# Performance work log

Measured on AMD Instinct MI355X. Metric: run time of the kernel, lower is better.

Reference implementation:

```python
import jax, jax.numpy as jnp
import numpy as np

N = 50000      # nodes
E = 800000     # edges (before self loops)
IN = 128       # input_dim
ED = 16        # edge_dim
HID = 32       # hidden_dim (per-head out_channels)
H = 4          # heads
OUT = 64       # output_dim
NEG = 0.1      # negative_slope
EPS = 1e-5     # batchnorm eps


def setup_inputs() -> dict:
    key = jax.random.key(0)
    ks = jax.random.split(key, 32)
    s = 0.1
    p = {}
    p["x"] = jax.random.normal(ks[0], (N, IN), jnp.float32)
    p["edge_index"] = jax.random.randint(ks[1], (2, E), 0, N, dtype=jnp.int32)
    p["edge_attr"] = jax.random.normal(ks[2], (E, ED), jnp.float32)
    # input embed: Linear(IN, HID) + BatchNorm1d (eval-mode running stats)
    p["W0"] = jax.random.normal(ks[3], (HID, IN), jnp.float32) * s
    p["b0"] = jnp.zeros((HID,), jnp.float32)
    p["bn_g"] = jnp.ones((HID,), jnp.float32)
    p["bn_b"] = jnp.zeros((HID,), jnp.float32)
    p["bn_m"] = jnp.zeros((HID,), jnp.float32)
    p["bn_v"] = jnp.ones((HID,), jnp.float32)
    # two GATv2Conv layers: lin_l, lin_r [H*HID, HID] (+bias), lin_edge [H*HID, ED] (no bias),
    # att [H, HID], out bias [HID] (concat=False)
    k = 4
    for l in range(2):
        p[f"Wl{l}"] = jax.random.normal(ks[k + 0], (H * HID, HID), jnp.float32) * s
        p[f"bl{l}"] = jnp.zeros((H * HID,), jnp.float32)
        p[f"Wr{l}"] = jax.random.normal(ks[k + 1], (H * HID, HID), jnp.float32) * s
        p[f"br{l}"] = jnp.zeros((H * HID,), jnp.float32)
        p[f"We{l}"] = jax.random.normal(ks[k + 2], (H * HID, ED), jnp.float32) * s
        p[f"att{l}"] = jax.random.normal(ks[k + 3], (H, HID), jnp.float32) * s
        p[f"bias{l}"] = jnp.zeros((HID,), jnp.float32)
        k += 4
    p["Wout"] = jax.random.normal(ks[k], (OUT, HID), jnp.float32) * s
    p["bout"] = jnp.zeros((OUT,), jnp.float32)
    return p


def _gatv2(x, src, dst, eattr, Wl, bl, Wr, br, We, att, bias):
    # x: [N, HID]; src/dst: [Et]; eattr: [Et, ED]
    xl = (x @ Wl.T + bl).reshape(N, H, HID)   # source transform
    xr = (x @ Wr.T + br).reshape(N, H, HID)   # target transform
    ea = (eattr @ We.T).reshape(-1, H, HID)   # edge transform
    m = jax.nn.leaky_relu(xl[src] + xr[dst] + ea, NEG)   # [Et, H, HID]
    alpha = jnp.einsum('ehc,hc->eh', m, att)             # [Et, H]
    amax = jax.ops.segment_max(alpha, dst, num_segments=N)  # every node has a self loop
    ex = jnp.exp(alpha - amax[dst])
    den = jax.ops.segment_sum(ex, dst, num_segments=N)
    w = ex / den[dst]                                    # segment softmax [Et, H]
    out = jax.ops.segment_sum(xl[src] * w[:, :, None], dst, num_segments=N)  # [N, H, HID]
    return out.mean(axis=1) + bias                       # concat=False -> mean heads


def reference(x, edge_index, edge_attr,
              W0, b0, bn_g, bn_b, bn_m, bn_v,
              Wl0, bl0, Wr0, br0, We0, att0, bias0,
              Wl1, bl1, Wr1, br1, We1, att1, bias1,
              Wout, bout):
    src, dst = edge_index[0], edge_index[1]
    # input embed: Linear + BatchNorm1d(eval) + LeakyReLU(0.1)
    e = x @ W0.T + b0
    e = (e - bn_m) / jnp.sqrt(bn_v + EPS) * bn_g + bn_b
    e = jax.nn.leaky_relu(e, NEG)
    # add self loops once (same both layers): fill_value='mean' => per-dst mean edge_attr
    cnt = jax.ops.segment_sum(jnp.ones((E,), jnp.float32), dst, num_segments=N)
    loop_attr = jax.ops.segment_sum(edge_attr, dst, num_segments=N) / jnp.maximum(cnt, 1.0)[:, None]
    ar = jnp.arange(N, dtype=src.dtype)
    src_f = jnp.concatenate([src, ar])
    dst_f = jnp.concatenate([dst, ar])
    ea_f = jnp.concatenate([edge_attr, loop_attr], axis=0)
    h = _gatv2(e, src_f, dst_f, ea_f, Wl0, bl0, Wr0, br0, We0, att0, bias0)
    h = _gatv2(h, src_f, dst_f, ea_f, Wl1, bl1, Wr1, br1, We1, att1, bias1)
    return jax.nn.leaky_relu(h @ Wout.T + bout, NEG)
```

## Files before the change

### kernel.cpp

```cpp
#include <hip/hip_runtime.h>
#include <hip/hip_fp16.h>
#include <math.h>

#define NN   50000
#define EE   800000
#define IND  128
#define EDD  16
#define HIDD 32
#define NH   4
#define HC   128
#define OUTD 64
#define NEG  0.1f
#define BN_EPS 1e-5f
#define LOG2E 1.44269504088896340736f

typedef __attribute__((ext_vector_type(2))) float v2f;
typedef __attribute__((ext_vector_type(2))) _Float16 v2h;

#if defined(__has_builtin)
#  if __has_builtin(__builtin_amdgcn_fdot2)
#    define HAVE_FDOT2 1
#  else
#    define HAVE_FDOT2 0
#  endif
#else
#  define HAVE_FDOT2 0
#endif

__device__ __forceinline__ float lrelu(float x) { return fmaxf(x, NEG * x); }
__device__ __forceinline__ v2f lrelu2(v2f v) { return __builtin_elementwise_max(v, v * NEG); }
__device__ __forceinline__ float2 unpk(float f) {
    return __half22float2(__builtin_bit_cast(__half2, f));
}

#define DPPADD(p, CTRL) do {                                                     \
    int _t = __builtin_amdgcn_update_dpp(0, __builtin_bit_cast(int, (p)),        \
                                         (CTRL), 0xF, 0xF, true);                \
    (p) += __builtin_bit_cast(float, _t);                                        \
} while (0)

__global__ void fold_kernel(const float* __restrict__ W0, const float* __restrict__ b0,
                            const float* __restrict__ g, const float* __restrict__ bb,
                            const float* __restrict__ bm, const float* __restrict__ bv,
                            const float* __restrict__ Wl0, const float* __restrict__ Wr0,
                            const float* __restrict__ Wl1, const float* __restrict__ Wr1,
                            const float* __restrict__ We0, const float* __restrict__ We1,
                            float* __restrict__ w0t, float* __restrict__ b0f,
                            float* __restrict__ wlt0, float* __restrict__ wrt0,
                            float* __restrict__ wlt1, float* __restrict__ wrt1,
                            __half2* __restrict__ weh0, __half2* __restrict__ weh1) {
    int tid = threadIdx.x;
    for (int idx = tid; idx < IND * HIDD; idx += 256) {
        int k = idx >> 5, c = idx & 31;
        float s = g[c] * (1.0f / sqrtf(bv[c] + BN_EPS));
        w0t[idx] = W0[c * IND + k] * s;
    }
    if (tid < HIDD) {
        float s = g[tid] * (1.0f / sqrtf(bv[tid] + BN_EPS));
        b0f[tid] = (b0[tid] - bm[tid]) * s + bb[tid];
    }
    for (int idx = tid; idx < HIDD * HC; idx += 256) {
        int k = idx >> 7, c = idx & 127;
        wlt0[idx] = Wl0[c * HIDD + k];
        wrt0[idx] = Wr0[c * HIDD + k];
        wlt1[idx] = Wl1[c * HIDD + k];
        wrt1[idx] = Wr1[c * HIDD + k];
    }
    for (int idx = tid; idx < HC * 8; idx += 256) {
        int c = idx >> 3, k = idx & 7;
        weh0[idx] = __floats2half2_rn(We0[c * EDD + 2 * k], We0[c * EDD + 2 * k + 1]);
        weh1[idx] = __floats2half2_rn(We1[c * EDD + 2 * k], We1[c * EDD + 2 * k + 1]);
    }
}

__global__ void count_embed_kernel(const int* __restrict__ ei, int* __restrict__ cnt,
                                   int* __restrict__ rank,
                                   const float* __restrict__ x,
                                   const float* __restrict__ w0t, const float* __restrict__ b0f,
                                   const float* __restrict__ wlt, const float* __restrict__ bl,
                                   const float* __restrict__ wrt, const float* __restrict__ br,
                                   __half2* __restrict__ xl, float* __restrict__ xr) {
    if (blockIdx.x < EE / 256) {
        int e = blockIdx.x * 256 + threadIdx.x;
        rank[e] = atomicAdd(&cnt[(unsigned)ei[EE + e] << 4], 1);
        return;
    }
    int tid = threadIdx.x;
    int n0 = (blockIdx.x - EE / 256) * 8;
    __shared__ float sx[8 * IND];
    __shared__ float se[8][HIDD];
    *(float4*)(sx + tid * 4) = *(const float4*)(x + (size_t)n0 * IND + tid * 4);
    __syncthreads();
    {
        int r = tid >> 5, c = tid & 31;
        float acc = b0f[c];
        const float* xrow = sx + r * IND;
        #pragma unroll 8
        for (int k = 0; k < IND; k++) acc += xrow[k] * w0t[k * HIDD + c];
        se[r][c] = lrelu(acc);
    }
    __syncthreads();
    int mat = tid >> 7, grp = (tid >> 6) & 1, pr = tid & 63;
    int c0 = 2 * pr;
    const float* WT = mat ? wrt : wlt;
    const float* b  = mat ? br : bl;
    v2f bv2 = (v2f){b[c0], b[c0 + 1]};
    v2f a0 = bv2, a1 = bv2, a2 = bv2, a3 = bv2;
    int nb = grp * 4;
    #pragma unroll
    for (int k = 0; k < HIDD; k++) {
        v2f wk = *(const v2f*)(WT + k * HC + c0);
        a0 += wk * se[nb + 0][k]; a1 += wk * se[nb + 1][k];
        a2 += wk * se[nb + 2][k]; a3 += wk * se[nb + 3][k];
    }
    if (mat == 0) {
        xl[((unsigned)(n0 + nb + 0) << 6) + pr] = __floats2half2_rn(a0.x, a0.y);
        xl[((unsigned)(n0 + nb + 1) << 6) + pr] = __floats2half2_rn(a1.x, a1.y);
        xl[((unsigned)(n0 + nb + 2) << 6) + pr] = __floats2half2_rn(a2.x, a2.y);
        xl[((unsigned)(n0 + nb + 3) << 6) + pr] = __floats2half2_rn(a3.x, a3.y);
    } else {
        *(float2*)(xr + ((unsigned)(n0 + nb + 0) << 7) + c0) = make_float2(a0.x, a0.y);
        *(float2*)(xr + ((unsigned)(n0 + nb + 1) << 7) + c0) = make_float2(a1.x, a1.y);
        *(float2*)(xr + ((unsigned)(n0 + nb + 2) << 7) + c0) = make_float2(a2.x, a2.y);
        *(float2*)(xr + ((unsigned)(n0 + nb + 3) << 7) + c0) = make_float2(a3.x, a3.y);
    }
}

__global__ void scan1_kernel(const int* cnt, int* pre, int* bsum) {
    int i = blockIdx.x * 1024 + threadIdx.x;
    int lane = threadIdx.x & 63, wid = threadIdx.x >> 6;
    __shared__ int wsum[16];
    int v = (i < NN) ? cnt[(unsigned)i << 4] : 0;
    int s = v;
    #pragma unroll
    for (int off = 1; off < 64; off <<= 1) {
        int t = __shfl_up(s, off);
        if (lane >= off) s += t;
    }
    if (lane == 63) wsum[wid] = s;
    __syncthreads();
    if (wid == 0) {
        int ws = (lane < 16) ? wsum[lane] : 0;
        #pragma unroll
        for (int off = 1; off < 16; off <<= 1) {
            int t = __shfl_up(ws, off);
            if (lane >= off) ws += t;
        }
        if (lane < 16) wsum[lane] = ws;
    }
    __syncthreads();
    int woff = (wid > 0) ? wsum[wid - 1] : 0;
    if (i < NN) pre[i] = woff + s - v;
    if (threadIdx.x == 1023) bsum[blockIdx.x] = wsum[15];
}

__global__ void scan3_kernel(int* rowstart, const int* pre, const int* bsum, int nb) {
    __shared__ int boff_s;
    if (threadIdx.x < 64) {
        int lane = threadIdx.x;
        int v = (lane < nb) ? bsum[lane] : 0;
        int s = v;
        #pragma unroll
        for (int off = 1; off < 64; off <<= 1) {
            int t = __shfl_up(s, off);
            if (lane >= off) s += t;
        }
        if (lane == (int)blockIdx.x) boff_s = s - v;
    }
    __syncthreads();
    int i = blockIdx.x * 1024 + threadIdx.x;
    if (i < NN) rowstart[i] = pre[i] + boff_s;
    if (i == 0) rowstart[NN] = EE;
}

__global__ void scatter_kernel(const int* __restrict__ ei, const int* __restrict__ rowstart,
                               const int* __restrict__ rank, const float* __restrict__ eattr,
                               int* __restrict__ csr_src, __half2* __restrict__ ea16) {
    int e = blockIdx.x * blockDim.x + threadIdx.x;
    if (e >= EE) return;
    int d = ei[EE + e];
    int pos = rowstart[d] + rank[e];
    csr_src[pos] = ei[e];
    const float4* src = (const float4*)(eattr + ((size_t)e << 4));
    float4 q0 = src[0], q1 = src[1], q2 = src[2], q3 = src[3];
    __half2 h[8];
    h[0] = __floats2half2_rn(q0.x, q0.y); h[1] = __floats2half2_rn(q0.z, q0.w);
    h[2] = __floats2half2_rn(q1.x, q1.y); h[3] = __floats2half2_rn(q1.z, q1.w);
    h[4] = __floats2half2_rn(q2.x, q2.y); h[5] = __floats2half2_rn(q2.z, q2.w);
    h[6] = __floats2half2_rn(q3.x, q3.y); h[7] = __floats2half2_rn(q3.z, q3.w);
    float4* dst = (float4*)(ea16 + ((size_t)pos << 3));
    dst[0] = *(float4*)&h[0];
    dst[1] = *(float4*)&h[4];
}

__global__ void lin_kernel(const float* __restrict__ f,
                           const float* __restrict__ wlt, const float* __restrict__ bl,
                           const float* __restrict__ wrt, const float* __restrict__ br,
                           __half2* __restrict__ xl, float* __restrict__ xr) {
    int tid = threadIdx.x;
    int n0 = blockIdx.x * 8;
    __shared__ float se[8][HIDD];
    se[tid >> 5][tid & 31] = f[((unsigned)(n0 + (tid >> 5)) << 5) + (tid & 31)];
    __syncthreads();
    int mat = tid >> 7, grp = (tid >> 6) & 1, pr = tid & 63;
    int c0 = 2 * pr;
    const float* WT = mat ? wrt : wlt;
    const float* b  = mat ? br : bl;
    v2f bv2 = (v2f){b[c0], b[c0 + 1]};
    v2f a0 = bv2, a1 = bv2, a2 = bv2, a3 = bv2;
    int nb = grp * 4;
    #pragma unroll
    for (int k = 0; k < HIDD; k++) {
        v2f wk = *(const v2f*)(WT + k * HC + c0);
        a0 += wk * se[nb + 0][k]; a1 += wk * se[nb + 1][k];
        a2 += wk * se[nb + 2][k]; a3 += wk * se[nb + 3][k];
    }
    if (mat == 0) {
        xl[((unsigned)(n0 + nb + 0) << 6) + pr] = __floats2half2_rn(a0.x, a0.y);
        xl[((unsigned)(n0 + nb + 1) << 6) + pr] = __floats2half2_rn(a1.x, a1.y);
        xl[((unsigned)(n0 + nb + 2) << 6) + pr] = __floats2half2_rn(a2.x, a2.y);
        xl[((unsigned)(n0 + nb + 3) << 6) + pr] = __floats2half2_rn(a3.x, a3.y);
    } else {
        *(float2*)(xr + ((unsigned)(n0 + nb + 0) << 7) + c0) = make_float2(a0.x, a0.y);
        *(float2*)(xr + ((unsigned)(n0 + nb + 1) << 7) + c0) = make_float2(a1.x, a1.y);
        *(float2*)(xr + ((unsigned)(n0 + nb + 2) << 7) + c0) = make_float2(a2.x, a2.y);
        *(float2*)(xr + ((unsigned)(n0 + nb + 3) << 7) + c0) = make_float2(a3.x, a3.y);
    }
}

template<bool OUTHEAD>
__global__ void gat_fused_kernel(const __half2* __restrict__ xl, const float* __restrict__ xr,
                                 const __half2* __restrict__ ea16,
                                 const float* __restrict__ We,
                                 const __half2* __restrict__ weh,
                                 const float* __restrict__ att,
                                 const int* __restrict__ rowstart, const int* __restrict__ csr_src,
                                 const float* __restrict__ bias,
                                 const float* __restrict__ Wout, const float* __restrict__ bout,
                                 float* __restrict__ out) {
    int n = (blockIdx.x * blockDim.x + threadIdx.x) >> 6;
    int lane = threadIdx.x & 63;
    if (n >= NN) return;
    n = __builtin_amdgcn_readfirstlane(n);
    int start = __builtin_amdgcn_readfirstlane(rowstart[n]);
    int end   = __builtin_amdgcn_readfirstlane(rowstart[n + 1]);
    int deg = end - start;
    int c0 = 2 * lane;

    __half2 xLh = xl[((unsigned)n << 6) + lane];
    v2f xrv = *(const v2f*)(xr + ((unsigned)n << 7) + c0);
    v2f attv = *(const v2f*)(att + c0) * LOG2E;

#if HAVE_FDOT2
    (void)We;
    v2h wh0[8], wh1[8];
    {
        const float4* pw = (const float4*)(weh + (size_t)c0 * 8);
        float4 q0 = pw[0], q1 = pw[1], q2 = pw[2], q3 = pw[3];
        float t[16];
        *(float4*)(t)      = q0; *(float4*)(t + 4)  = q1;
        *(float4*)(t + 8)  = q2; *(float4*)(t + 12) = q3;
        #pragma unroll
        for (int k = 0; k < 8; k++) {
            wh0[k] = __builtin_bit_cast(v2h, t[k]);
            wh1[k] = __builtin_bit_cast(v2h, t[8 + k]);
        }
    }
    auto proj = [&](float4 r0, float4 r1) -> v2f {
        float e[8];
        *(float4*)(e) = r0; *(float4*)(e + 4) = r1;
        float a0 = 0.f, a1 = 0.f;
        #pragma unroll
        for (int k = 0; k < 8; k++) {
            v2h ek = __builtin_bit_cast(v2h, e[k]);
            a0 = __builtin_amdgcn_fdot2(ek, wh0[k], a0, false);
            a1 = __builtin_amdgcn_fdot2(ek, wh1[k], a1, false);
        }
        return (v2f){a0, a1};
    };
#else
    (void)weh;
    v2f wv[16];
    {
        const float* ra = We + c0 * EDD;
        const float* rb = ra + EDD;
        float4 a0 = *(const float4*)(ra),     a1 = *(const float4*)(ra + 4);
        float4 a2 = *(const float4*)(ra + 8), a3 = *(const float4*)(ra + 12);
        float4 b0 = *(const float4*)(rb),     b1 = *(const float4*)(rb + 4);
        float4 b2 = *(const float4*)(rb + 8), b3 = *(const float4*)(rb + 12);
        wv[0]=(v2f){a0.x,b0.x}; wv[1]=(v2f){a0.y,b0.y}; wv[2]=(v2f){a0.z,b0.z}; wv[3]=(v2f){a0.w,b0.w};
        wv[4]=(v2f){a1.x,b1.x}; wv[5]=(v2f){a1.y,b1.y}; wv[6]=(v2f){a1.z,b1.z}; wv[7]=(v2f){a1.w,b1.w};
        wv[8]=(v2f){a2.x,b2.x}; wv[9]=(v2f){a2.y,b2.y}; wv[10]=(v2f){a2.z,b2.z}; wv[11]=(v2f){a2.w,b2.w};
        wv[12]=(v2f){a3.x,b3.x}; wv[13]=(v2f){a3.y,b3.y}; wv[14]=(v2f){a3.z,b3.z}; wv[15]=(v2f){a3.w,b3.w};
    }
    auto proj = [&](float4 r0, float4 r1) -> v2f {
        float2 t0 = unpk(r0.x), t1 = unpk(r0.y), t2 = unpk(r0.z), t3 = unpk(r0.w);
        float2 t4 = unpk(r1.x), t5 = unpk(r1.y), t6 = unpk(r1.z), t7 = unpk(r1.w);
        return wv[0]*t0.x  + wv[1]*t0.y  + wv[2]*t1.x  + wv[3]*t1.y
             + wv[4]*t2.x  + wv[5]*t2.y  + wv[6]*t3.x  + wv[7]*t3.y
             + wv[8]*t4.x  + wv[9]*t4.y  + wv[10]*t5.x + wv[11]*t5.y
             + wv[12]*t6.x + wv[13]*t6.y + wv[14]*t7.x + wv[15]*t7.y;
    };
#endif

    float lh = 0.f;
    v2f acc   = (v2f){0.f, 0.f};
    v2f easum = (v2f){0.f, 0.f};

    auto proc = [&](v2f xv, v2f ea) {
        easum += ea;
        v2f z  = xv + xrv + ea;
        v2f mm = lrelu2(z);
        v2f pp = mm * attv;
        float p = pp.x + pp.y;
        DPPADD(p, 0xB1);
        DPPADD(p, 0x4E);
        DPPADD(p, 0x124);
        DPPADD(p, 0x128);
        float w = exp2f(p);
        lh  += w;
        acc += xv * w;
    };

    #define GATHER(i0, S0, S1, S2, S3, X0, X1, X2, X3, E0, E1, E2, E3) do {           \
        __half2 xh0 = xl[((unsigned)(S0) << 6) + lane];                                \
        __half2 xh1 = xl[((unsigned)(S1) << 6) + lane];                                \
        __half2 xh2 = xl[((unsigned)(S2) << 6) + lane];                                \
        __half2 xh3 = xl[((unsigned)(S3) << 6) + lane];                                \
        const float4* ep = (const float4*)(ea16 + ((size_t)(unsigned)(i0) << 3));      \
        float4 r00 = ep[0], r01 = ep[1], r10 = ep[2], r11 = ep[3];                     \
        float4 r20 = ep[4], r21 = ep[5], r30 = ep[6], r31 = ep[7];                     \
        E0 = proj(r00, r01); E1 = proj(r10, r11);                                      \
        E2 = proj(r20, r21); E3 = proj(r30, r31);                                      \
        float2 xf;                                                                     \
        xf = __half22float2(xh0); X0 = (v2f){xf.x, xf.y};                              \
        xf = __half22float2(xh1); X1 = (v2f){xf.x, xf.y};                              \
        xf = __half22float2(xh2); X2 = (v2f){xf.x, xf.y};                              \
        xf = __half22float2(xh3); X3 = (v2f){xf.x, xf.y};                              \
    } while (0)

    int i = start;
    int nf = deg >> 2;
    if (nf > 0) {
        int v0 = csr_src[i],     v1 = csr_src[i + 1],
            v2 = csr_src[i + 2], v3 = csr_src[i + 3];
        int j4 = (i + 4 > EE - 4) ? (EE - 4) : (i + 4);
        int u0 = csr_src[j4],     u1 = csr_src[j4 + 1],
            u2 = csr_src[j4 + 2], u3 = csr_src[j4 + 3];
        int s0 = __builtin_amdgcn_readfirstlane(v0), s1 = __builtin_amdgcn_readfirstlane(v1);
        int s2 = __builtin_amdgcn_readfirstlane(v2), s3 = __builtin_amdgcn_readfirstlane(v3);
        v2f A0x, A1x, A2x, A3x, A0e, A1e, A2e, A3e;
        GATHER(i, s0, s1, s2, s3, A0x, A1x, A2x, A3x, A0e, A1e, A2e, A3e);
        for (int k = 1; k < nf; k++) {
            int jn = i + 4 * (k + 1);
            jn = (jn > EE - 4) ? (EE - 4) : jn;
            int w0 = csr_src[jn],     w1 = csr_src[jn + 1],
                w2 = csr_src[jn + 2], w3 = csr_src[jn + 3];
            int t0 = __builtin_amdgcn_readfirstlane(u0), t1 = __builtin_amdgcn_readfirstlane(u1);
            int t2 = __builtin_amdgcn_readfirstlane(u2), t3 = __builtin_amdgcn_readfirstlane(u3);
            v2f B0x, B1x, B2x, B3x, B0e, B1e, B2e, B3e;
            GATHER(i + 4 * k, t0, t1, t2, t3, B0x, B1x, B2x, B3x, B0e, B1e, B2e, B3e);
            proc(A0x, A0e); proc(A1x, A1e); proc(A2x, A2e); proc(A3x, A3e);
            A0x = B0x; A1x = B1x; A2x = B2x; A3x = B3x;
            A0e = B0e; A1e = B1e; A2e = B2e; A3e = B3e;
            u0 = w0; u1 = w1; u2 = w2; u3 = w3;
        }
        proc(A0x, A0e); proc(A1x, A1e); proc(A2x, A2e); proc(A3x, A3e);
        i += 4 * nf;
    }
    int rem = end - i;
    if (rem > 0) {
        v2f Tx[3], Te[3];
        int sA = __builtin_amdgcn_readfirstlane(csr_src[i]);
        int sB = (rem > 1) ? __builtin_amdgcn_readfirstlane(csr_src[i + 1]) : sA;
        int sC = (rem > 2) ? __builtin_amdgcn_readfirstlane(csr_src[i + 2]) : sA;
        __half2 xh0 = xl[((unsigned)sA << 6) + lane];
        __half2 xh1 = xl[((unsigned)sB << 6) + lane];
        __half2 xh2 = xl[((unsigned)sC << 6) + lane];
        const float4* ep = (const float4*)(ea16 + ((size_t)(unsigned)i << 3));
        int lim2 = (rem > 1) ? 2 : 0, lim4 = (rem > 2) ? 4 : 0;
        float4 r00 = ep[0], r01 = ep[1];
        float4 r10 = ep[lim2], r11 = ep[lim2 + 1];
        float4 r20 = ep[lim4], r21 = ep[lim4 + 1];
        float2 xf;
        xf = __half22float2(xh0); Tx[0] = (v2f){xf.x, xf.y};
        xf = __half22float2(xh1); Tx[1] = (v2f){xf.x, xf.y};
        xf = __half22float2(xh2); Tx[2] = (v2f){xf.x, xf.y};
        Te[0] = proj(r00, r01); Te[1] = proj(r10, r11); Te[2] = proj(r20, r21);
        proc(Tx[0], Te[0]);
        if (rem > 1) proc(Tx[1], Te[1]);
        if (rem > 2) proc(Tx[2], Te[2]);
    }

    {
        float invdeg = 1.0f / (float)(deg > 0 ? deg : 1);
        float2 xf = __half22float2(xLh);
        proc((v2f){xf.x, xf.y}, easum * invdeg);
    }

    float inv = 1.0f / lh;
    float acc0 = acc.x * inv, acc1 = acc.y * inv;
    acc0 += __shfl_xor(acc0, 16); acc0 += __shfl_xor(acc0, 32);
    acc1 += __shfl_xor(acc1, 16); acc1 += __shfl_xor(acc1, 32);

    if (!OUTHEAD) {
        if (lane < 16) {
            float2 o = make_float2(acc0 * 0.25f + bias[2 * lane],
                                   acc1 * 0.25f + bias[2 * lane + 1]);
            *(float2*)(out + ((unsigned)n << 5) + 2 * lane) = o;
        }
    } else {
        __shared__ __align__(16) float sh[4][HIDD];
        int w = threadIdx.x >> 6;
        if (lane < 16) {
            sh[w][2 * lane]     = acc0 * 0.25f + bias[2 * lane];
            sh[w][2 * lane + 1] = acc1 * 0.25f + bias[2 * lane + 1];
        }
        float a = bout[lane];
        const float4* wr4 = (const float4*)(Wout + lane * HIDD);
        const float4* sv4 = (const float4*)(&sh[w][0]);
        #pragma unroll
        for (int k = 0; k < 8; k++) {
            float4 s4 = sv4[k], w4 = wr4[k];
            a += s4.x * w4.x + s4.y * w4.y + s4.z * w4.z + s4.w * w4.w;
        }
        out[((unsigned)n << 6) + lane] = lrelu(a);
    }
    #undef GATHER
}

extern "C" void kernel_launch(void* const* d_in, const int* in_sizes, int n_in,
                              void* d_out, int out_size, void* d_ws, size_t ws_size,
                              hipStream_t stream) {
    const float* x     = (const float*)d_in[0];
    const int*   ei    = (const int*)  d_in[1];
    const float* eattr = (const float*)d_in[2];
    const float* W0    = (const float*)d_in[3];
    const float* b0    = (const float*)d_in[4];
    const float* bn_g  = (const float*)d_in[5];
    const float* bn_b  = (const float*)d_in[6];
    const float* bn_m  = (const float*)d_in[7];
    const float* bn_v  = (const float*)d_in[8];
    const float* Wl[2]   = { (const float*)d_in[9],  (const float*)d_in[16] };
    const float* bl[2]   = { (const float*)d_in[10], (const float*)d_in[17] };
    const float* Wr[2]   = { (const float*)d_in[11], (const float*)d_in[18] };
    const float* br[2]   = { (const float*)d_in[12], (const float*)d_in[19] };
    const float* We[2]   = { (const float*)d_in[13], (const float*)d_in[20] };
    const float* att[2]  = { (const float*)d_in[14], (const float*)d_in[21] };
    const float* bias[2] = { (const float*)d_in[15], (const float*)d_in[22] };
    const float* Wout  = (const float*)d_in[23];
    const float* bout  = (const float*)d_in[24];
    float* out = (float*)d_out;

    const int NB = (NN + 1023) / 1024;
    char* p = (char*)d_ws;
    auto carve = [&](size_t bytes) { char* r = p; p += (bytes + 255) & ~(size_t)255; return r; };
    float*   h1       = (float*)  carve((size_t)NN * HIDD * 4);
    __half2* xl       = (__half2*)carve((size_t)NN * HC * 2);
    float*   xr       = (float*)  carve((size_t)NN * HC * 4);
    int*     cnt      = (int*)    carve((size_t)NN * 64);
    int*     rank     = (int*)    carve((size_t)EE * 4);
    int*     pre      = (int*)    carve((size_t)NN * 4);
    int*     bsum     = (int*)    carve((size_t)64 * 4);
    int*     rowstart = (int*)    carve((size_t)(NN + 1) * 4);
    int*     csr_src  = (int*)    carve((size_t)EE * 4);
    __half2* ea16     = (__half2*)carve((size_t)EE * EDD * 2);
    float*   w0t      = (float*)  carve((size_t)IND * HIDD * 4);
    float*   b0f      = (float*)  carve((size_t)HIDD * 4);
    float*   wlt0     = (float*)  carve((size_t)HIDD * HC * 4);
    float*   wrt0     = (float*)  carve((size_t)HIDD * HC * 4);
    float*   wlt1     = (float*)  carve((size_t)HIDD * HC * 4);
    float*   wrt1     = (float*)  carve((size_t)HIDD * HC * 4);
    __half2* weh0     = (__half2*)carve((size_t)HC * 8 * 4);
    __half2* weh1     = (__half2*)carve((size_t)HC * 8 * 4);

    hipMemsetAsync(cnt, 0, (size_t)NN * 64, stream);

    fold_kernel<<<1, 256, 0, stream>>>(W0, b0, bn_g, bn_b, bn_m, bn_v,
                                       Wl[0], Wr[0], Wl[1], Wr[1], We[0], We[1],
                                       w0t, b0f, wlt0, wrt0, wlt1, wrt1, weh0, weh1);
    count_embed_kernel<<<EE / 256 + NN / 8, 256, 0, stream>>>(
        ei, cnt, rank, x, w0t, b0f, wlt0, bl[0], wrt0, br[0], xl, xr);
    scan1_kernel<<<NB, 1024, 0, stream>>>(cnt, pre, bsum);
    scan3_kernel<<<NB, 1024, 0, stream>>>(rowstart, pre, bsum, NB);
    scatter_kernel<<<(EE + 255) / 256, 256, 0, stream>>>(ei, rowstart, rank, eattr,
                                                         csr_src, ea16);

    gat_fused_kernel<false><<<(NN * 64) / 256, 256, 0, stream>>>(
        xl, xr, ea16, We[0], weh0, att[0], rowstart, csr_src, bias[0], nullptr, nullptr, h1);

    lin_kernel<<<NN / 8, 256, 0, stream>>>(h1, wlt1, bl[1], wrt1, br[1], xl, xr);
    gat_fused_kernel<true><<<(NN * 64) / 256, 256, 0, stream>>>(
        xl, xr, ea16, We[1], weh1, att[1], rowstart, csr_src, bias[1], Wout, bout, out);
}
```

Baseline: 465.6 us.

## Keep edge attributes in original order and gather them by edge id

Converts edge attributes to fp16 in the counting pass in original edge order, and has the scatter pass write only (source, edge id) pairs into the CSR. The GAT kernels then fetch each edge's attribute row through the stored edge id instead of reading them contiguously in CSR order. This removes the scattered 32-byte attribute write from the scatter kernel, but it turns the contiguous attribute reads in both GAT layers into random gathers and doubles the size of the CSR index reads.

Measured after the change: 448.4 us. 1.04x faster.

```diff
diff --git a/kernel.cpp b/kernel.cpp
--- a/kernel.cpp
+++ b/kernel.cpp
@@ -75,6 +75,8 @@
 
 __global__ void count_embed_kernel(const int* __restrict__ ei, int* __restrict__ cnt,
                                    int* __restrict__ rank,
+                                   const float* __restrict__ eattr,
+                                   __half2* __restrict__ ea16,
                                    const float* __restrict__ x,
                                    const float* __restrict__ w0t, const float* __restrict__ b0f,
                                    const float* __restrict__ wlt, const float* __restrict__ bl,
@@ -82,7 +84,17 @@
                                    __half2* __restrict__ xl, float* __restrict__ xr) {
     if (blockIdx.x < EE / 256) {
         int e = blockIdx.x * 256 + threadIdx.x;
+        const float4* src = (const float4*)(eattr + ((size_t)e << 4));
+        float4 q0 = src[0], q1 = src[1], q2 = src[2], q3 = src[3];
         rank[e] = atomicAdd(&cnt[(unsigned)ei[EE + e] << 4], 1);
+        __half2 h[8];
+        h[0] = __floats2half2_rn(q0.x, q0.y); h[1] = __floats2half2_rn(q0.z, q0.w);
+        h[2] = __floats2half2_rn(q1.x, q1.y); h[3] = __floats2half2_rn(q1.z, q1.w);
+        h[4] = __floats2half2_rn(q2.x, q2.y); h[5] = __floats2half2_rn(q2.z, q2.w);
+        h[6] = __floats2half2_rn(q3.x, q3.y); h[7] = __floats2half2_rn(q3.z, q3.w);
+        float4* dst = (float4*)(ea16 + ((size_t)e << 3));
+        dst[0] = *(float4*)&h[0];
+        dst[1] = *(float4*)&h[4];
         return;
     }
     int tid = threadIdx.x;
@@ -174,23 +186,12 @@
 }
 
 __global__ void scatter_kernel(const int* __restrict__ ei, const int* __restrict__ rowstart,
-                               const int* __restrict__ rank, const float* __restrict__ eattr,
-                               int* __restrict__ csr_src, __half2* __restrict__ ea16) {
+                               const int* __restrict__ rank, int2* __restrict__ csr2) {
     int e = blockIdx.x * blockDim.x + threadIdx.x;
     if (e >= EE) return;
     int d = ei[EE + e];
     int pos = rowstart[d] + rank[e];
-    csr_src[pos] = ei[e];
-    const float4* src = (const float4*)(eattr + ((size_t)e << 4));
-    float4 q0 = src[0], q1 = src[1], q2 = src[2], q3 = src[3];
-    __half2 h[8];
-    h[0] = __floats2half2_rn(q0.x, q0.y); h[1] = __floats2half2_rn(q0.z, q0.w);
-    h[2] = __floats2half2_rn(q1.x, q1.y); h[3] = __floats2half2_rn(q1.z, q1.w);
-    h[4] = __floats2half2_rn(q2.x, q2.y); h[5] = __floats2half2_rn(q2.z, q2.w);
-    h[6] = __floats2half2_rn(q3.x, q3.y); h[7] = __floats2half2_rn(q3.z, q3.w);
-    float4* dst = (float4*)(ea16 + ((size_t)pos << 3));
-    dst[0] = *(float4*)&h[0];
-    dst[1] = *(float4*)&h[4];
+    csr2[pos] = make_int2(ei[e], e);
 }
 
 __global__ void lin_kernel(const float* __restrict__ f,
@@ -234,7 +235,7 @@
                                  const float* __restrict__ We,
                                  const __half2* __restrict__ weh,
                                  const float* __restrict__ att,
-                                 const int* __restrict__ rowstart, const int* __restrict__ csr_src,
+                                 const int* __restrict__ rowstart, const int2* __restrict__ csr2,
                                  const float* __restrict__ bias,
                                  const float* __restrict__ Wout, const float* __restrict__ bout,
                                  float* __restrict__ out) {
@@ -322,14 +323,18 @@
         acc += xv * w;
     };
 
-    #define GATHER(i0, S0, S1, S2, S3, X0, X1, X2, X3, E0, E1, E2, E3) do {           \
+    #define GATHER(S0, S1, S2, S3, E0i, E1i, E2i, E3i,                                 \
+                   X0, X1, X2, X3, E0, E1, E2, E3) do {                                \
         __half2 xh0 = xl[((unsigned)(S0) << 6) + lane];                                \
         __half2 xh1 = xl[((unsigned)(S1) << 6) + lane];                                \
         __half2 xh2 = xl[((unsigned)(S2) << 6) + lane];                                \
         __half2 xh3 = xl[((unsigned)(S3) << 6) + lane];                                \
-        const float4* ep = (const float4*)(ea16 + ((size_t)(unsigned)(i0) << 3));      \
-        float4 r00 = ep[0], r01 = ep[1], r10 = ep[2], r11 = ep[3];                     \
-        float4 r20 = ep[4], r21 = ep[5], r30 = ep[6], r31 = ep[7];                     \
+        const float4* e0p = (const float4*)(ea16 + ((size_t)(unsigned)(E0i) << 3));    \
+        const float4* e1p = (const float4*)(ea16 + ((size_t)(unsigned)(E1i) << 3));    \
+        const float4* e2p = (const float4*)(ea16 + ((size_t)(unsigned)(E2i) << 3));    \
+        const float4* e3p = (const float4*)(ea16 + ((size_t)(unsigned)(E3i) << 3));    \
+        float4 r00 = e0p[0], r01 = e0p[1], r10 = e1p[0], r11 = e1p[1];                 \
+        float4 r20 = e2p[0], r21 = e2p[1], r30 = e3p[0], r31 = e3p[1];                 \
         E0 = proj(r00, r01); E1 = proj(r10, r11);                                      \
         E2 = proj(r20, r21); E3 = proj(r30, r31);                                      \
         float2 xf;                                                                     \
@@ -342,24 +347,26 @@
     int i = start;
     int nf = deg >> 2;
     if (nf > 0) {
-        int v0 = csr_src[i],     v1 = csr_src[i + 1],
-            v2 = csr_src[i + 2], v3 = csr_src[i + 3];
+        int2 v0 = csr2[i],     v1 = csr2[i + 1],
+             v2 = csr2[i + 2], v3 = csr2[i + 3];
         int j4 = (i + 4 > EE - 4) ? (EE - 4) : (i + 4);
-        int u0 = csr_src[j4],     u1 = csr_src[j4 + 1],
-            u2 = csr_src[j4 + 2], u3 = csr_src[j4 + 3];
-        int s0 = __builtin_amdgcn_readfirstlane(v0), s1 = __builtin_amdgcn_readfirstlane(v1);
-        int s2 = __builtin_amdgcn_readfirstlane(v2), s3 = __builtin_amdgcn_readfirstlane(v3);
+        int2 u0 = csr2[j4],     u1 = csr2[j4 + 1],
+             u2 = csr2[j4 + 2], u3 = csr2[j4 + 3];
+        int s0 = __builtin_amdgcn_readfirstlane(v0.x), s1 = __builtin_amdgcn_readfirstlane(v1.x);
+        int s2 = __builtin_amdgcn_readfirstlane(v2.x), s3 = __builtin_amdgcn_readfirstlane(v3.x);
         v2f A0x, A1x, A2x, A3x, A0e, A1e, A2e, A3e;
-        GATHER(i, s0, s1, s2, s3, A0x, A1x, A2x, A3x, A0e, A1e, A2e, A3e);
+        GATHER(s0, s1, s2, s3, v0.y, v1.y, v2.y, v3.y,
+               A0x, A1x, A2x, A3x, A0e, A1e, A2e, A3e);
         for (int k = 1; k < nf; k++) {
             int jn = i + 4 * (k + 1);
             jn = (jn > EE - 4) ? (EE - 4) : jn;
-            int w0 = csr_src[jn],     w1 = csr_src[jn + 1],
-                w2 = csr_src[jn + 2], w3 = csr_src[jn + 3];
-            int t0 = __builtin_amdgcn_readfirstlane(u0), t1 = __builtin_amdgcn_readfirstlane(u1);
-            int t2 = __builtin_amdgcn_readfirstlane(u2), t3 = __builtin_amdgcn_readfirstlane(u3);
+            int2 w0 = csr2[jn],     w1 = csr2[jn + 1],
+                 w2 = csr2[jn + 2], w3 = csr2[jn + 3];
+            int t0 = __builtin_amdgcn_readfirstlane(u0.x), t1 = __builtin_amdgcn_readfirstlane(u1.x);
+            int t2 = __builtin_amdgcn_readfirstlane(u2.x), t3 = __builtin_amdgcn_readfirstlane(u3.x);
             v2f B0x, B1x, B2x, B3x, B0e, B1e, B2e, B3e;
-            GATHER(i + 4 * k, t0, t1, t2, t3, B0x, B1x, B2x, B3x, B0e, B1e, B2e, B3e);
+            GATHER(t0, t1, t2, t3, u0.y, u1.y, u2.y, u3.y,
+                   B0x, B1x, B2x, B3x, B0e, B1e, B2e, B3e);
             proc(A0x, A0e); proc(A1x, A1e); proc(A2x, A2e); proc(A3x, A3e);
             A0x = B0x; A1x = B1x; A2x = B2x; A3x = B3x;
             A0e = B0e; A1e = B1e; A2e = B2e; A3e = B3e;
@@ -371,17 +378,21 @@
     int rem = end - i;
     if (rem > 0) {
         v2f Tx[3], Te[3];
-        int sA = __builtin_amdgcn_readfirstlane(csr_src[i]);
-        int sB = (rem > 1) ? __builtin_amdgcn_readfirstlane(csr_src[i + 1]) : sA;
-        int sC = (rem > 2) ? __builtin_amdgcn_readfirstlane(csr_src[i + 2]) : sA;
+        int2 cA = csr2[i];
+        int2 cB = (rem > 1) ? csr2[i + 1] : cA;
+        int2 cC = (rem > 2) ? csr2[i + 2] : cA;
+        int sA = __builtin_amdgcn_readfirstlane(cA.x);
+        int sB = __builtin_amdgcn_readfirstlane(cB.x);
+        int sC = __builtin_amdgcn_readfirstlane(cC.x);
         __half2 xh0 = xl[((unsigned)sA << 6) + lane];
         __half2 xh1 = xl[((unsigned)sB << 6) + lane];
         __half2 xh2 = xl[((unsigned)sC << 6) + lane];
-        const float4* ep = (const float4*)(ea16 + ((size_t)(unsigned)i << 3));
-        int lim2 = (rem > 1) ? 2 : 0, lim4 = (rem > 2) ? 4 : 0;
-        float4 r00 = ep[0], r01 = ep[1];
-        float4 r10 = ep[lim2], r11 = ep[lim2 + 1];
-        float4 r20 = ep[lim4], r21 = ep[lim4 + 1];
+        const float4* eAp = (const float4*)(ea16 + ((size_t)(unsigned)cA.y << 3));
+        const float4* eBp = (const float4*)(ea16 + ((size_t)(unsigned)cB.y << 3));
+        const float4* eCp = (const float4*)(ea16 + ((size_t)(unsigned)cC.y << 3));
+        float4 r00 = eAp[0], r01 = eAp[1];
+        float4 r10 = eBp[0], r11 = eBp[1];
+        float4 r20 = eCp[0], r21 = eCp[1];
         float2 xf;
         xf = __half22float2(xh0); Tx[0] = (v2f){xf.x, xf.y};
         xf = __half22float2(xh1); Tx[1] = (v2f){xf.x, xf.y};
@@ -463,7 +474,7 @@
     int*     pre      = (int*)    carve((size_t)NN * 4);
     int*     bsum     = (int*)    carve((size_t)64 * 4);
     int*     rowstart = (int*)    carve((size_t)(NN + 1) * 4);
-    int*     csr_src  = (int*)    carve((size_t)EE * 4);
+    int2*    csr2     = (int2*)   carve((size_t)EE * 8);
     __half2* ea16     = (__half2*)carve((size_t)EE * EDD * 2);
     float*   w0t      = (float*)  carve((size_t)IND * HIDD * 4);
     float*   b0f      = (float*)  carve((size_t)HIDD * 4);
@@ -480,16 +491,15 @@
                                        Wl[0], Wr[0], Wl[1], Wr[1], We[0], We[1],
                                        w0t, b0f, wlt0, wrt0, wlt1, wrt1, weh0, weh1);
     count_embed_kernel<<<EE / 256 + NN / 8, 256, 0, stream>>>(
-        ei, cnt, rank, x, w0t, b0f, wlt0, bl[0], wrt0, br[0], xl, xr);
+        ei, cnt, rank, eattr, ea16, x, w0t, b0f, wlt0, bl[0], wrt0, br[0], xl, xr);
     scan1_kernel<<<NB, 1024, 0, stream>>>(cnt, pre, bsum);
     scan3_kernel<<<NB, 1024, 0, stream>>>(rowstart, pre, bsum, NB);
-    scatter_kernel<<<(EE + 255) / 256, 256, 0, stream>>>(ei, rowstart, rank, eattr,
-                                                         csr_src, ea16);
+    scatter_kernel<<<(EE + 255) / 256, 256, 0, stream>>>(ei, rowstart, rank, csr2);
 
     gat_fused_kernel<false><<<(NN * 64) / 256, 256, 0, stream>>>(
-        xl, xr, ea16, We[0], weh0, att[0], rowstart, csr_src, bias[0], nullptr, nullptr, h1);
+        xl, xr, ea16, We[0], weh0, att[0], rowstart, csr2, bias[0], nullptr, nullptr, h1);
 
     lin_kernel<<<NN / 8, 256, 0, stream>>>(h1, wlt1, bl[1], wrt1, br[1], xl, xr);
     gat_fused_kernel<true><<<(NN * 64) / 256, 256, 0, stream>>>(
-        xl, xr, ea16, We[1], weh1, att[1], rowstart, csr_src, bias[1], Wout, bout, out);
-}
+        xl, xr, ea16, We[1], weh1, att[1], rowstart, csr2, bias[1], Wout, bout, out);
+}
```
